# Performance work log

Measured on AMD Instinct MI355X. Metric: run time of the kernel, lower is better.

## Reference

```python
import jax, jax.numpy as jnp
import numpy as np

N_NODES = 50000
N_EDGES = 600000
IN_DIM, HID_DIM, OUT_DIM = 128, 256, 40


def setup_inputs() -> dict:
    key = jax.random.key(0)
    ks = jax.random.split(key, 10)
    x = jax.random.normal(ks[0], (N_NODES, IN_DIM), dtype=jnp.float32)
    edge_index = jax.random.randint(ks[1], (2, N_EDGES), 0, N_NODES, dtype=jnp.int64)
    def lin(k, out_d, in_d):
        s = 1.0 / np.sqrt(in_d)
        return jax.random.uniform(k, (out_d, in_d), jnp.float32, -s, s)
    # SAGEConv: lin_l (on aggregated neighbors, with bias) + lin_r (on self, no bias)
    params = {
        "Wl1": lin(ks[2], HID_DIM, IN_DIM), "bl1": jnp.zeros((HID_DIM,), jnp.float32), "Wr1": lin(ks[3], HID_DIM, IN_DIM),
        "Wl2": lin(ks[4], HID_DIM, HID_DIM), "bl2": jnp.zeros((HID_DIM,), jnp.float32), "Wr2": lin(ks[5], HID_DIM, HID_DIM),
        "Wl3": lin(ks[6], OUT_DIM, HID_DIM), "bl3": jnp.zeros((OUT_DIM,), jnp.float32), "Wr3": lin(ks[7], OUT_DIM, HID_DIM),
    }
    return {"x": x, "edge_index": edge_index, **params}


def _sage_conv(x, src, dst, Wl, bl, Wr):
    # mean-aggregate source features into destination nodes
    n = x.shape[0]
    agg = jax.ops.segment_sum(x[src], dst, num_segments=n)          # [N, d_in]
    cnt = jax.ops.segment_sum(jnp.ones_like(dst, dtype=x.dtype), dst, num_segments=n)
    mean = agg / jnp.maximum(cnt, 1.0)[:, None]
    return mean @ Wl.T + bl + x @ Wr.T


def reference(x, edge_index, Wl1, bl1, Wr1, Wl2, bl2, Wr2, Wl3, bl3, Wr3):
    src, dst = edge_index[0], edge_index[1]
    h = _sage_conv(x, src, dst, Wl1, bl1, Wr1)
    h = jax.nn.relu(h)  # dropout is identity in eval mode
    h = _sage_conv(h, src, dst, Wl2, bl2, Wr2)
    h = jax.nn.relu(h)
    h = _sage_conv(h, src, dst, Wl3, bl3, Wr3)
    return jax.nn.log_softmax(h, axis=1)
```

## Files before the change

### kernel.cpp

```cpp
#include <hip/hip_runtime.h>
#include <hip/hip_bf16.h>

#define IN_DIM 128
#define HID_DIM 256
#define OUT_DIM 40
#define SCAN_CHUNK 2048

typedef __attribute__((ext_vector_type(8))) __bf16 bf16x8;
typedef __attribute__((ext_vector_type(4))) float f32x4;

__device__ inline ushort f2bf(float f) {
    uint u = __builtin_bit_cast(uint, f);
    u = (u + 0x7fff + ((u >> 16) & 1)) >> 16;
    return (ushort)u;
}
__device__ inline float bfl(uint u) { return __builtin_bit_cast(float, u << 16); }
__device__ inline float bfh(uint u) { return __builtin_bit_cast(float, u & 0xffff0000u); }

__global__ __launch_bounds__(256) void prep_kernel(
    const float* __restrict__ x, ushort* __restrict__ xb, int n4, int XB,
    const float* __restrict__ Wl1, const float* __restrict__ Wr1,
    const float* __restrict__ Wl2, const float* __restrict__ Wr2,
    const float* __restrict__ Wl3, const float* __restrict__ Wr3,
    ushort* __restrict__ o1l, ushort* __restrict__ o1r,
    ushort* __restrict__ o2l, ushort* __restrict__ o2r,
    ushort* __restrict__ o3l, ushort* __restrict__ o3r, int WB,
    const int* __restrict__ dst, int* __restrict__ cnt, int E) {
    int b = blockIdx.x;
    if (b < XB) {
        int i = b * 256 + threadIdx.x;
        if (i < n4) {
            float4 v = ((const float4*)x)[i];
            uint2 o;
            o.x = (uint)f2bf(v.x) | ((uint)f2bf(v.y) << 16);
            o.y = (uint)f2bf(v.z) | ((uint)f2bf(v.w) << 16);
            ((uint2*)xb)[i] = o;
        }
        return;
    }
    b -= XB;
    if (b < WB) {
        int idx = b * 256 + threadIdx.x;
        if (idx < 32768) {
            int j = idx & 7, ln = (idx >> 3) & 15, quad = (idx >> 7) & 3;
            int kk = (idx >> 9) & 3, ct = (idx >> 11) & 3, cb = idx >> 13;
            int o = cb * 64 + ct * 16 + ln;
            int k = kk * 32 + quad * 8 + j;
            o1l[idx] = f2bf(Wl1[o * 128 + k]);
            o1r[idx] = f2bf(Wr1[o * 128 + k]);
            return;
        }
        idx -= 32768;
        if (idx < 65536) {
            int j = idx & 7, ln = (idx >> 3) & 15, quad = (idx >> 7) & 3;
            int kk = (idx >> 9) & 7, ct = (idx >> 12) & 3, cb = idx >> 14;
            int o = cb * 64 + ct * 16 + ln;
            int k = kk * 32 + quad * 8 + j;
            o2l[idx] = f2bf(Wl2[o * 256 + k]);
            o2r[idx] = f2bf(Wr2[o * 256 + k]);
            return;
        }
        idx -= 65536;
        if (idx < 48 * 256) {
            int row = idx >> 8;
            int col = idx & 255;
            ushort vl = 0, vr = 0;
            if (row < OUT_DIM) {
                vl = f2bf(Wl3[row * 256 + col]);
                vr = f2bf(Wr3[row * 256 + col]);
            }
            o3l[idx] = vl;
            o3r[idx] = vr;
        }
        return;
    }
    b -= WB;
    int e = b * 256 + threadIdx.x;
    if (e < E) atomicAdd(&cnt[dst[e]], 1);
}

__global__ __launch_bounds__(256) void scan_pass1(const int* __restrict__ cnt,
                                                  int* __restrict__ bsum, int N) {
    __shared__ int red[256];
    const int base = blockIdx.x * SCAN_CHUNK;
    int s = 0;
    for (int i = threadIdx.x; i < SCAN_CHUNK; i += 256) {
        int idx = base + i;
        if (idx < N) s += cnt[idx];
    }
    red[threadIdx.x] = s;
    __syncthreads();
    for (int o = 128; o > 0; o >>= 1) {
        if (threadIdx.x < o) red[threadIdx.x] += red[threadIdx.x + o];
        __syncthreads();
    }
    if (threadIdx.x == 0) bsum[blockIdx.x] = red[0];
}

__global__ __launch_bounds__(256) void scan_pass3(const int* __restrict__ cnt,
                                                  const int* __restrict__ bsum,
                                                  int* __restrict__ rowptr,
                                                  int* __restrict__ cursor,
                                                  float* __restrict__ inv,
                                                  int N, int E, int SB) {
    __shared__ int ls[256];
    __shared__ int boff;
    if (threadIdx.x == 0) {
        int r = 0;
        for (int i = 0; i < blockIdx.x; ++i) r += bsum[i];
        boff = r;
    }
    const int tbase = blockIdx.x * SCAN_CHUNK + threadIdx.x * 8;
    int c[8];
    int s = 0;
#pragma unroll
    for (int j = 0; j < 8; ++j) {
        int idx = tbase + j;
        c[j] = (idx < N) ? cnt[idx] : 0;
        s += c[j];
    }
    ls[threadIdx.x] = s;
    __syncthreads();
    for (int o = 1; o < 256; o <<= 1) {
        int u = (threadIdx.x >= o) ? ls[threadIdx.x - o] : 0;
        __syncthreads();
        ls[threadIdx.x] += u;
        __syncthreads();
    }
    int run = boff + ls[threadIdx.x] - s;
#pragma unroll
    for (int j = 0; j < 8; ++j) {
        int idx = tbase + j;
        if (idx < N) {
            rowptr[idx] = run;
            cursor[idx] = run;
            inv[idx] = 1.0f / fmaxf((float)c[j], 1.0f);
            run += c[j];
        }
    }
    if (blockIdx.x == 0 && threadIdx.x == 0) rowptr[N] = E;
}

__global__ __launch_bounds__(256) void fill_kernel(const int* __restrict__ src,
                                                   const int* __restrict__ dst,
                                                   int* __restrict__ cursor,
                                                   int* __restrict__ srcs, int E) {
    int e = blockIdx.x * 256 + threadIdx.x;
    if (e < E) {
        int pos = atomicAdd(&cursor[dst[e]], 1);
        srcs[pos] = src[e];
    }
}

template <int D>
__global__ __launch_bounds__(256) void gather_mean_bf(const ushort* __restrict__ feat,
                                                      const int* __restrict__ rowptr,
                                                      const int* __restrict__ srcs,
                                                      const float* __restrict__ inv,
                                                      ushort* __restrict__ out, int N) {
    constexpr int V = D / 64;
    const int wave = threadIdx.x >> 6;
    const int lane = threadIdx.x & 63;
    const int n = blockIdx.x * 4 + wave;
    if (n >= N) return;
    const int beg = rowptr[n];
    const int end = rowptr[n + 1];
    const int col = lane * V;
    float a0 = 0.f, a1 = 0.f, a2 = 0.f, a3 = 0.f;
    int e = beg;
    if constexpr (V == 4) {
        for (; e + 7 < end; e += 8) {
            uint2 q[8];
#pragma unroll
            for (int j = 0; j < 8; ++j)
                q[j] = *(const uint2*)&feat[(long long)srcs[e + j] * D + col];
#pragma unroll
            for (int j = 0; j < 8; ++j) {
                a0 += bfl(q[j].x); a1 += bfh(q[j].x);
                a2 += bfl(q[j].y); a3 += bfh(q[j].y);
            }
        }
        for (; e + 3 < end; e += 4) {
            uint2 q[4];
#pragma unroll
            for (int j = 0; j < 4; ++j)
                q[j] = *(const uint2*)&feat[(long long)srcs[e + j] * D + col];
#pragma unroll
            for (int j = 0; j < 4; ++j) {
                a0 += bfl(q[j].x); a1 += bfh(q[j].x);
                a2 += bfl(q[j].y); a3 += bfh(q[j].y);
            }
        }
        for (; e < end; ++e) {
            uint2 q0 = *(const uint2*)&feat[(long long)srcs[e] * D + col];
            a0 += bfl(q0.x); a1 += bfh(q0.x); a2 += bfl(q0.y); a3 += bfh(q0.y);
        }
        const float sc = inv[n];
        uint2 o;
        o.x = (uint)f2bf(a0 * sc) | ((uint)f2bf(a1 * sc) << 16);
        o.y = (uint)f2bf(a2 * sc) | ((uint)f2bf(a3 * sc) << 16);
        *(uint2*)&out[(long long)n * D + col] = o;
    } else {
        for (; e + 7 < end; e += 8) {
            uint q[8];
#pragma unroll
            for (int j = 0; j < 8; ++j)
                q[j] = *(const uint*)&feat[(long long)srcs[e + j] * D + col];
#pragma unroll
            for (int j = 0; j < 8; ++j) {
                a0 += bfl(q[j]); a1 += bfh(q[j]);
            }
        }
        for (; e + 3 < end; e += 4) {
            uint q[4];
#pragma unroll
            for (int j = 0; j < 4; ++j)
                q[j] = *(const uint*)&feat[(long long)srcs[e + j] * D + col];
#pragma unroll
            for (int j = 0; j < 4; ++j) {
                a0 += bfl(q[j]); a1 += bfh(q[j]);
            }
        }
        for (; e < end; ++e) {
            uint q0 = *(const uint*)&feat[(long long)srcs[e] * D + col];
            a0 += bfl(q0); a1 += bfh(q0);
        }
        const float sc = inv[n];
        uint o = (uint)f2bf(a0 * sc) | ((uint)f2bf(a1 * sc) << 16);
        *(uint*)&out[(long long)n * D + col] = o;
    }
}

template <int K, bool RELU, bool OUTBF>
__global__ __launch_bounds__(256, 3) void sage_gemm_mfma(const ushort* __restrict__ Amean,
                                                         const ushort* __restrict__ Aself,
                                                         const ushort* __restrict__ Wl,
                                                         const float* __restrict__ bias,
                                                         const ushort* __restrict__ Wr,
                                                         void* __restrict__ outv, int N, int O) {
    constexpr int NK = K / 32;
    constexpr int TILE = 64 * K;

    const int tid = threadIdx.x;
    const int wave = tid >> 6;
    const int lane = tid & 63;
    const int ln = lane & 15;
    const int quad = lane >> 4;
    const int bm0 = blockIdx.y * 128;
    const int cb = blockIdx.x;

    int arow[2];
#pragma unroll
    for (int rt = 0; rt < 2; ++rt) {
        int r = bm0 + wave * 32 + rt * 16 + ln;
        arow[rt] = min(r, N - 1);
    }

    f32x4 acc[2][4] = {};

#pragma unroll
    for (int p = 0; p < 2; ++p) {
        const ushort* __restrict__ A = p ? Aself : Amean;
        const ushort* __restrict__ Wfrag = (p ? Wr : Wl) + (size_t)cb * TILE + lane * 8;

        bf16x8 areg[NK][2];
#pragma unroll
        for (int kk = 0; kk < NK; ++kk)
#pragma unroll
            for (int rt = 0; rt < 2; ++rt)
                areg[kk][rt] = *(const bf16x8*)&A[(long long)arow[rt] * K + kk * 32 + quad * 8];

#pragma unroll
        for (int kk = 0; kk < NK; ++kk) {
#pragma unroll
            for (int ct = 0; ct < 4; ++ct) {
                bf16x8 b = *(const bf16x8*)&Wfrag[(ct * NK + kk) * 512];
#pragma unroll
                for (int rt = 0; rt < 2; ++rt)
                    acc[rt][ct] = __builtin_amdgcn_mfma_f32_16x16x32_bf16(areg[kk][rt], b, acc[rt][ct], 0, 0, 0);
            }
        }
    }

#pragma unroll
    for (int rt = 0; rt < 2; ++rt) {
        int rbase = bm0 + wave * 32 + rt * 16 + quad * 4;
#pragma unroll
        for (int ct = 0; ct < 4; ++ct) {
            int col = cb * 64 + ct * 16 + ln;
            if (col >= O) continue;
            float bv = bias[col];
#pragma unroll
            for (int r = 0; r < 4; ++r) {
                int row = rbase + r;
                if (row >= N) continue;
                float v = acc[rt][ct][r] + bv;
                if (RELU) v = fmaxf(v, 0.f);
                if (OUTBF)
                    ((ushort*)outv)[(long long)row * O + col] = f2bf(v);
                else
                    ((float*)outv)[(long long)row * O + col] = v;
            }
        }
    }
}

template <int K>
__global__ __launch_bounds__(256, 3) void sage_gemm_pre(const ushort* __restrict__ A0,
                                                        const ushort* __restrict__ Wl,
                                                        const ushort* __restrict__ Wr,
                                                        ushort* __restrict__ P,
                                                        float* __restrict__ S, int N, int O) {
    constexpr int KP = 2 * K + 8;
    constexpr int NK = K / 32;
    __shared__ __align__(16) ushort Ws[48 * KP];

    const int tid = threadIdx.x;
    const int wave = tid >> 6;
    const int lane = tid & 63;
    const int ln = lane & 15;
    const int quad = lane >> 4;
    const int bm0 = blockIdx.x * 64;

    const int arow = min(bm0 + wave * 16 + ln, N - 1);

#pragma unroll
    for (int i = tid; i < 48 * (K / 8); i += 256) {
        int row = i / (K / 8);
        int c8 = (i % (K / 8)) * 8;
        *(ulonglong2*)&Ws[row * KP + c8] =
            *(const ulonglong2*)&Wl[(long long)row * K + c8];
        *(ulonglong2*)&Ws[row * KP + K + c8] =
            *(const ulonglong2*)&Wr[(long long)row * K + c8];
    }
    __syncthreads();

#pragma unroll
    for (int phase = 0; phase < 2; ++phase) {
        f32x4 acc[3] = {};
#pragma unroll
        for (int kk = 0; kk < NK; ++kk) {
            bf16x8 a = *(const bf16x8*)&A0[(long long)arow * K + kk * 32 + quad * 8];
#pragma unroll
            for (int ct = 0; ct < 3; ++ct) {
                bf16x8 b = *(const bf16x8*)&Ws[(ct * 16 + ln) * KP + phase * K + kk * 32 + quad * 8];
                acc[ct] = __builtin_amdgcn_mfma_f32_16x16x32_bf16(a, b, acc[ct], 0, 0, 0);
            }
        }
        int rbase = bm0 + wave * 16 + quad * 4;
#pragma unroll
        for (int ct = 0; ct < 3; ++ct) {
            int col = ct * 16 + ln;
            if (col >= O) continue;
#pragma unroll
            for (int r = 0; r < 4; ++r) {
                int row = rbase + r;
                if (row >= N) continue;
                if (phase == 0)
                    P[(long long)row * O + col] = f2bf(acc[ct][r]);
                else
                    S[(long long)row * O + col] = acc[ct][r];
            }
        }
    }
}

__global__ __launch_bounds__(256) void agg_bias_lsm(const ushort* __restrict__ P,
                                                    const float* __restrict__ S,
                                                    const float* __restrict__ bias,
                                                    const int* __restrict__ rowptr,
                                                    const int* __restrict__ srcs,
                                                    const float* __restrict__ inv,
                                                    float* __restrict__ out, int N) {
    const int wave = threadIdx.x >> 6;
    const int lane = threadIdx.x & 63;
    const int n = blockIdx.x * 4 + wave;
    if (n >= N) return;
    const int beg = rowptr[n];
    const int end = rowptr[n + 1];
    const bool act = lane < OUT_DIM;
    const int cidx = act ? lane : 0;

    float acc = 0.f;
    int e = beg;
    for (; e + 3 < end; e += 4) {
        int s0 = srcs[e], s1 = srcs[e + 1], s2 = srcs[e + 2], s3 = srcs[e + 3];
        float v0 = __builtin_bit_cast(float, (uint)P[(long long)s0 * OUT_DIM + cidx] << 16);
        float v1 = __builtin_bit_cast(float, (uint)P[(long long)s1 * OUT_DIM + cidx] << 16);
        float v2 = __builtin_bit_cast(float, (uint)P[(long long)s2 * OUT_DIM + cidx] << 16);
        float v3 = __builtin_bit_cast(float, (uint)P[(long long)s3 * OUT_DIM + cidx] << 16);
        acc += (v0 + v1) + (v2 + v3);
    }
    for (; e < end; ++e)
        acc += __builtin_bit_cast(float, (uint)P[(long long)srcs[e] * OUT_DIM + cidx] << 16);

    float v = act ? (acc * inv[n] + S[(long long)n * OUT_DIM + lane] + bias[lane]) : -INFINITY;
    float m = v;
#pragma unroll
    for (int o = 32; o > 0; o >>= 1) m = fmaxf(m, __shfl_xor(m, o, 64));
    float ex = act ? expf(v - m) : 0.f;
    float sm = ex;
#pragma unroll
    for (int o = 32; o > 0; o >>= 1) sm += __shfl_xor(sm, o, 64);
    float ls = logf(sm);
    if (act) out[(long long)n * OUT_DIM + lane] = v - m - ls;
}

extern "C" void kernel_launch(void* const* d_in, const int* in_sizes, int n_in,
                              void* d_out, int out_size, void* d_ws, size_t ws_size,
                              hipStream_t stream) {
    const float* x   = (const float*)d_in[0];
    const int*   ei  = (const int*)d_in[1];
    const float* Wl1 = (const float*)d_in[2];
    const float* bl1 = (const float*)d_in[3];
    const float* Wr1 = (const float*)d_in[4];
    const float* Wl2 = (const float*)d_in[5];
    const float* bl2 = (const float*)d_in[6];
    const float* Wr2 = (const float*)d_in[7];
    const float* Wl3 = (const float*)d_in[8];
    const float* bl3 = (const float*)d_in[9];
    const float* Wr3 = (const float*)d_in[10];
    float* out = (float*)d_out;

    const int N = in_sizes[0] / IN_DIM;
    const int E = in_sizes[1] / 2;
    const int* src = ei;
    const int* dst = ei + E;

    char* w = (char*)d_ws;
    size_t off = 0;
    auto alloc = [&](size_t bytes) {
        void* p = w + off;
        off = (off + bytes + 255) & ~(size_t)255;
        return p;
    };
    ushort* xb   = (ushort*)alloc((size_t)N * IN_DIM * 2);
    ushort* M    = (ushort*)alloc((size_t)N * HID_DIM * 2);
    ushort* H1   = (ushort*)alloc((size_t)N * HID_DIM * 2);
    ushort* H2   = (ushort*)alloc((size_t)N * HID_DIM * 2);
    ushort* P3   = (ushort*)alloc((size_t)N * OUT_DIM * 2);
    float*  S3   = (float*)alloc((size_t)N * OUT_DIM * 4);
    float*  inv  = (float*)alloc((size_t)N * 4);
    int*    cnt  = (int*)alloc((size_t)N * 4);
    int*    rowptr = (int*)alloc((size_t)(N + 1) * 4);
    int*    cursor = (int*)alloc((size_t)N * 4);
    int*    srcs = (int*)alloc((size_t)E * 4);
    int*    bsum = (int*)alloc(256 * 4);
    ushort* Wl1b = (ushort*)alloc(256 * 128 * 2);
    ushort* Wr1b = (ushort*)alloc(256 * 128 * 2);
    ushort* Wl2b = (ushort*)alloc(256 * 256 * 2);
    ushort* Wr2b = (ushort*)alloc(256 * 256 * 2);
    ushort* Wl3b = (ushort*)alloc(48 * 256 * 2);
    ushort* Wr3b = (ushort*)alloc(48 * 256 * 2);

    const int n4 = N * IN_DIM / 4;
    const int XB = (n4 + 255) / 256;
    const int WB = (32768 + 65536 + 48 * 256 + 255) / 256;
    const int HB = (E + 255) / 256;
    hipMemsetAsync(cnt, 0, (size_t)N * sizeof(int), stream);
    prep_kernel<<<XB + WB + HB, 256, 0, stream>>>(
        x, xb, n4, XB,
        Wl1, Wr1, Wl2, Wr2, Wl3, Wr3,
        Wl1b, Wr1b, Wl2b, Wr2b, Wl3b, Wr3b, WB,
        dst, cnt, E);

    const int SB = (N + SCAN_CHUNK - 1) / SCAN_CHUNK;
    scan_pass1<<<SB, 256, 0, stream>>>(cnt, bsum, N);
    scan_pass3<<<SB, 256, 0, stream>>>(cnt, bsum, rowptr, cursor, inv, N, E, SB);
    fill_kernel<<<HB, 256, 0, stream>>>(src, dst, cursor, srcs, E);

    const int gm = (N + 127) / 128;
    const int gg = (N + 3) / 4;

    gather_mean_bf<IN_DIM><<<gg, 256, 0, stream>>>(xb, rowptr, srcs, inv, M, N);
    sage_gemm_mfma<IN_DIM, true, true><<<dim3(4, gm), 256, 0, stream>>>(
        M, xb, Wl1b, bl1, Wr1b, H1, N, HID_DIM);

    gather_mean_bf<HID_DIM><<<gg, 256, 0, stream>>>(H1, rowptr, srcs, inv, M, N);
    sage_gemm_mfma<HID_DIM, true, true><<<dim3(4, gm), 256, 0, stream>>>(
        M, H1, Wl2b, bl2, Wr2b, H2, N, HID_DIM);

    sage_gemm_pre<HID_DIM><<<(N + 63) / 64, 256, 0, stream>>>(
        H2, Wl3b, Wr3b, P3, S3, N, OUT_DIM);
    agg_bias_lsm<<<gg, 256, 0, stream>>>(P3, S3, bl3, rowptr, srcs, inv, out, N);
}
```

Measured before the change: 365.3 us.

## Stage GEMM weight tiles in LDS via direct global-to-LDS loads with XCD swizzle

The SAGE MFMA GEMM now copies each block's weight tile into shared memory with global_load_lds, and all waves read B fragments from LDS instead of each wave loading them from global/L2. The grid is flattened to 1D and block IDs are remapped so consecutive logical tiles land on the same XCD, aiming for better L2 reuse of A rows across the four column blocks. The occupancy hint rises from 3 to 4 blocks per CU. The cost is added barriers and LDS usage (up to 32 KB for K=256), which may cap occupancy below the requested level.

New measurement: 345.7 us. -5.4%, faster.

```diff
diff --git a/kernel.cpp b/kernel.cpp
--- a/kernel.cpp
+++ b/kernel.cpp
@@ -16,6 +16,17 @@
 }
 __device__ inline float bfl(uint u) { return __builtin_bit_cast(float, u << 16); }
 __device__ inline float bfh(uint u) { return __builtin_bit_cast(float, u & 0xffff0000u); }
+
+__device__ inline void gload_lds16(const ushort* g, ushort* l) {
+    __builtin_amdgcn_global_load_lds((const __attribute__((address_space(1))) void*)g,
+                                     (__attribute__((address_space(3))) void*)l, 16, 0, 0);
+}
+
+__device__ inline int xcd_swizzle(int b, int G) {
+    int q = G >> 3, r = G & 7;
+    int xcd = b & 7, j = b >> 3;
+    return (xcd < r ? xcd * (q + 1) : r * (q + 1) + (xcd - r) * q) + j;
+}
 
 __global__ __launch_bounds__(256) void prep_kernel(
     const float* __restrict__ x, ushort* __restrict__ xb, int n4, int XB,
@@ -232,22 +243,27 @@
 }
 
 template <int K, bool RELU, bool OUTBF>
-__global__ __launch_bounds__(256, 3) void sage_gemm_mfma(const ushort* __restrict__ Amean,
+__global__ __launch_bounds__(256, 4) void sage_gemm_mfma(const ushort* __restrict__ Amean,
                                                          const ushort* __restrict__ Aself,
                                                          const ushort* __restrict__ Wl,
                                                          const float* __restrict__ bias,
                                                          const ushort* __restrict__ Wr,
-                                                         void* __restrict__ outv, int N, int O) {
+                                                         void* __restrict__ outv, int N, int O,
+                                                         int G) {
     constexpr int NK = K / 32;
     constexpr int TILE = 64 * K;
+    constexpr int CHUNKS = TILE / 512;
+    __shared__ __align__(16) ushort Ws[TILE];
 
     const int tid = threadIdx.x;
     const int wave = tid >> 6;
     const int lane = tid & 63;
     const int ln = lane & 15;
     const int quad = lane >> 4;
-    const int bm0 = blockIdx.y * 128;
-    const int cb = blockIdx.x;
+
+    const int wid = xcd_swizzle(blockIdx.x, G);
+    const int cb = wid & 3;
+    const int bm0 = (wid >> 2) * 128;
 
     int arow[2];
 #pragma unroll
@@ -261,7 +277,12 @@
 #pragma unroll
     for (int p = 0; p < 2; ++p) {
         const ushort* __restrict__ A = p ? Aself : Amean;
-        const ushort* __restrict__ Wfrag = (p ? Wr : Wl) + (size_t)cb * TILE + lane * 8;
+        const ushort* __restrict__ gsrc = (p ? Wr : Wl) + (size_t)cb * TILE;
+
+        if (p) __syncthreads();
+#pragma unroll
+        for (int c = wave; c < CHUNKS; c += 4)
+            gload_lds16(gsrc + c * 512 + lane * 8, &Ws[c * 512]);
 
         bf16x8 areg[NK][2];
 #pragma unroll
@@ -270,11 +291,13 @@
             for (int rt = 0; rt < 2; ++rt)
                 areg[kk][rt] = *(const bf16x8*)&A[(long long)arow[rt] * K + kk * 32 + quad * 8];
 
+        __syncthreads();
+
 #pragma unroll
         for (int kk = 0; kk < NK; ++kk) {
 #pragma unroll
             for (int ct = 0; ct < 4; ++ct) {
-                bf16x8 b = *(const bf16x8*)&Wfrag[(ct * NK + kk) * 512];
+                bf16x8 b = *(const bf16x8*)&Ws[((ct * NK + kk) * 64 + lane) * 8];
 #pragma unroll
                 for (int rt = 0; rt < 2; ++rt)
                     acc[rt][ct] = __builtin_amdgcn_mfma_f32_16x16x32_bf16(areg[kk][rt], b, acc[rt][ct], 0, 0, 0);
@@ -470,15 +493,16 @@
     fill_kernel<<<HB, 256, 0, stream>>>(src, dst, cursor, srcs, E);
 
     const int gm = (N + 127) / 128;
+    const int G = 4 * gm;
     const int gg = (N + 3) / 4;
 
     gather_mean_bf<IN_DIM><<<gg, 256, 0, stream>>>(xb, rowptr, srcs, inv, M, N);
-    sage_gemm_mfma<IN_DIM, true, true><<<dim3(4, gm), 256, 0, stream>>>(
-        M, xb, Wl1b, bl1, Wr1b, H1, N, HID_DIM);
+    sage_gemm_mfma<IN_DIM, true, true><<<G, 256, 0, stream>>>(
+        M, xb, Wl1b, bl1, Wr1b, H1, N, HID_DIM, G);
 
     gather_mean_bf<HID_DIM><<<gg, 256, 0, stream>>>(H1, rowptr, srcs, inv, M, N);
-    sage_gemm_mfma<HID_DIM, true, true><<<dim3(4, gm), 256, 0, stream>>>(
-        M, H1, Wl2b, bl2, Wr2b, H2, N, HID_DIM);
+    sage_gemm_mfma<HID_DIM, true, true><<<G, 256, 0, stream>>>(
+        M, H1, Wl2b, bl2, Wr2b, H2, N, HID_DIM, G);
 
     sage_gemm_pre<HID_DIM><<<(N + 63) / 64, 256, 0, stream>>>(
         H2, Wl3b, Wr3b, P3, S3, N, OUT_DIM);
```
